# Optimization experiments

Measured on AMD Instinct MI355X. Metric: run time of the kernel, lower is better.

Reference implementation:

```python
import jax, jax.numpy as jnp
import numpy as np

MIN_K = 1
MAX_K = 10


def setup_inputs() -> dict:
    key = jax.random.key(0)
    k1, k2 = jax.random.split(key)
    query_features = jax.random.normal(k1, (256, 256, 32, 32), dtype=jnp.float32)
    support_features = jax.random.normal(k2, (512, 256, 32, 32), dtype=jnp.float32)
    return {"query_features": query_features, "support_features": support_features}


def _pairwise_euclidean(q, s):
    # torch.cdist(p=2): sqrt(||q||^2 + ||s||^2 - 2 q.s)
    q2 = jnp.sum(q * q, axis=1, keepdims=True)            # [Nq, 1]
    s2 = jnp.sum(s * s, axis=1)                           # [Ns]
    d2 = q2 + s2[None, :] - 2.0 * (q @ s.T)               # [Nq, Ns]
    return jnp.sqrt(jnp.maximum(d2, 0.0))


def reference(query_features, support_features):
    Nq = query_features.shape[0]
    q = query_features.reshape(Nq, -1)                    # [Nq, D]
    s = support_features.reshape(support_features.shape[0], -1)  # [Ns, D]

    dist = _pairwise_euclidean(q, s)                      # [Nq, Ns]

    # One top-k at MAX_K replaces the redundant per-k cdist+topk loop:
    # the per-k "loss" in optimize_k is mean of the k smallest-distance INDICES,
    # which is order-invariant, so prefix sums over sorted top-k suffice.
    _, idx = jax.lax.top_k(-dist, MAX_K)                  # [Nq, MAX_K] indices of k-NN (ascending distance)
    idx_f = idx.astype(jnp.float32)

    prefix = jnp.cumsum(jnp.sum(idx_f, axis=0))           # [MAX_K] sum of indices over first k cols
    ks = jnp.arange(1, MAX_K + 1, dtype=jnp.float32)
    losses = prefix / (Nq * ks)                           # mean index for each k
    best_k = jnp.argmin(losses[MIN_K - 1:]) + MIN_K       # traced scalar in [MIN_K, MAX_K]

    # threshold = mean of knn indices at best_k
    kmask = (jnp.arange(MAX_K) < best_k).astype(jnp.float32)  # [MAX_K]
    threshold = jnp.sum(idx_f * kmask[None, :]) / (Nq * best_k.astype(jnp.float32))

    # high_similarity mask: original expands [Nq, k] -> [Nq, D] (valid iff k==1),
    # i.e. a per-query boolean from the nearest-neighbor index vs threshold.
    qmask = (idx_f[:, 0] < threshold)                     # [Nq]

    # Original does data-dependent boolean gather; for static shapes we apply the
    # mask multiplicatively (zero out filtered queries).
    refined = q * qmask[:, None].astype(q.dtype)          # [Nq, D]
    return refined
```

## Files before the change

### kernel.cpp

```cpp
#include <hip/hip_runtime.h>
#include <cstdint>


typedef __attribute__((ext_vector_type(8))) __bf16 bf16x8;
typedef __attribute__((ext_vector_type(4))) float f32x4;
typedef __attribute__((ext_vector_type(4))) unsigned int uintx4;

#define KTOT 262144
#define MQ 256
#define NS 512
#define KSPLIT 128
#define KC 2048
#define BK 32
#define NSTEPS 64
#define BBASE 32768
#define BUFB 65536

__device__ inline unsigned int cvtpk_bf16(float a, float b) {
    unsigned int r;
    asm("v_cvt_pk_bf16_f32 %0, %1, %2" : "=v"(r) : "v"(a), "v"(b));
    return r;
}

__device__ inline void split2(float a, float b, unsigned int& h, unsigned int& l) {
    h = cvtpk_bf16(a, b);
    float ra = a - __uint_as_float(h << 16);
    float rb = b - __uint_as_float(h & 0xFFFF0000u);
    l = cvtpk_bf16(ra, rb);
}

__device__ inline void split8u(const float4& x, const float4& y, uintx4& h, uintx4& l) {
    unsigned int h0, h1, h2, h3, l0, l1, l2, l3;
    split2(x.x, x.y, h0, l0);
    split2(x.z, x.w, h1, l1);
    split2(y.x, y.y, h2, l2);
    split2(y.z, y.w, h3, l3);
    h = (uintx4){h0, h1, h2, h3};
    l = (uintx4){l0, l1, l2, l3};
}

#define LDF(OFF) (*(const bf16x8*)&Lds[(OFF)])

#define MM(MI, AH, AL, BH, BL, J)                                                        \
    acc[MI][J] = __builtin_amdgcn_mfma_f32_16x16x32_bf16(AH, BH, acc[MI][J], 0, 0, 0);   \
    acc[MI][J] = __builtin_amdgcn_mfma_f32_16x16x32_bf16(AH, BL, acc[MI][J], 0, 0, 0);   \
    acc[MI][J] = __builtin_amdgcn_mfma_f32_16x16x32_bf16(AL, BH, acc[MI][J], 0, 0, 0);

#define MMROW(MI, AH, AL)                                                                \
    MM(MI, AH, AL, bh0, bl0, 0) MM(MI, AH, AL, bh1, bl1, 1)                              \
    MM(MI, AH, AL, bh2, bl2, 2) MM(MI, AH, AL, bh3, bl3, 3)

__global__ __launch_bounds__(512, 2)
void k1_gemm(const float* __restrict__ Q, const float* __restrict__ S,
             float* __restrict__ Ppart, float* __restrict__ s2part)
{
    __shared__ __align__(16) unsigned char Lds[2 * BUFB];

    const int tid  = threadIdx.x;
    const int lane = tid & 63;
    const int w    = tid >> 6;
    const int wm   = w >> 2;
    const int wn   = w & 3;
    const int lr   = lane & 15;
    const int lk   = lane >> 4;

    const int phys  = blockIdx.x;
    const int xcd   = phys & 7;
    const int ord   = phys >> 3;
    const int chunk = xcd * 16 + (ord >> 1);
    const int ntile = ord & 1;
    const long k0   = (long)chunk * KC;

    const int rowh = tid >> 1;
    const int h    = tid & 1;
    const int e    = rowh & 7;
    const float* qsrc = Q + (long)rowh * KTOT + k0 + h * 16;
    const float* ssrc = S + (long)(ntile * 256 + rowh) * KTOT + k0 + h * 16;
    const int aw0 = rowh * 128 + (((2 * h + 0) ^ e) * 16);
    const int aw1 = rowh * 128 + (((2 * h + 1) ^ e) * 16);
    const int aw2 = rowh * 128 + (((2 * h + 4) ^ e) * 16);
    const int aw3 = rowh * 128 + (((2 * h + 5) ^ e) * 16);

    const int e2  = lr & 7;
    const int aHi = (wm * 128 + lr) * 128 + ((lk ^ e2) * 16);
    const int aLo = (wm * 128 + lr) * 128 + (((lk + 4) ^ e2) * 16);
    const int bHi = BBASE + (wn * 64 + lr) * 128 + ((lk ^ e2) * 16);
    const int bLo = BBASE + (wn * 64 + lr) * 128 + (((lk + 4) ^ e2) * 16);

    f32x4 acc[8][4];
#pragma unroll
    for (int i = 0; i < 8; ++i)
#pragma unroll
        for (int j = 0; j < 4; ++j)
            acc[i][j] = (f32x4){0.f, 0.f, 0.f, 0.f};

    float ssq = 0.f;
    float4 pa0, pa1, pa2, pa3, pb0, pb1, pb2, pb3;

#define LOADREGS {                                                         \
    pa0 = *(const float4*)(qsrc);      pa1 = *(const float4*)(qsrc + 4);   \
    pa2 = *(const float4*)(qsrc + 8);  pa3 = *(const float4*)(qsrc + 12);  \
    pb0 = *(const float4*)(ssrc);      pb1 = *(const float4*)(ssrc + 4);   \
    pb2 = *(const float4*)(ssrc + 8);  pb3 = *(const float4*)(ssrc + 12);  \
    qsrc += BK; ssrc += BK; }

#define SPLITSTORE(BASE) {                                                 \
    uintx4 u0, u1, u2, u3, v0, v1, v2, v3;                                 \
    split8u(pa0, pa1, u0, v0);                                             \
    split8u(pa2, pa3, u1, v1);                                             \
    split8u(pb0, pb1, u2, v2);                                             \
    split8u(pb2, pb3, u3, v3);                                             \
    ssq += pb0.x*pb0.x + pb0.y*pb0.y + pb0.z*pb0.z + pb0.w*pb0.w           \
         + pb1.x*pb1.x + pb1.y*pb1.y + pb1.z*pb1.z + pb1.w*pb1.w           \
         + pb2.x*pb2.x + pb2.y*pb2.y + pb2.z*pb2.z + pb2.w*pb2.w           \
         + pb3.x*pb3.x + pb3.y*pb3.y + pb3.z*pb3.z + pb3.w*pb3.w;          \
    *(uintx4*)&Lds[(BASE) + aw0] = u0;                                     \
    *(uintx4*)&Lds[(BASE) + aw1] = u1;                                     \
    *(uintx4*)&Lds[(BASE) + aw2] = v0;                                     \
    *(uintx4*)&Lds[(BASE) + aw3] = v1;                                     \
    *(uintx4*)&Lds[(BASE) + BBASE + aw0] = u2;                             \
    *(uintx4*)&Lds[(BASE) + BBASE + aw1] = u3;                             \
    *(uintx4*)&Lds[(BASE) + BBASE + aw2] = v2;                             \
    *(uintx4*)&Lds[(BASE) + BBASE + aw3] = v3; }

    LOADREGS
    SPLITSTORE(0)
    LOADREGS
    asm volatile("s_waitcnt lgkmcnt(0)" ::: "memory");
    __builtin_amdgcn_s_barrier();
    __builtin_amdgcn_sched_barrier(0);

    for (int s = 0; s < NSTEPS; ++s) {
        const int cur = (s & 1) * BUFB;
        const int nxt = cur ^ BUFB;

        if (s + 1 < NSTEPS) SPLITSTORE(nxt)
        if (s + 2 < NSTEPS) LOADREGS

        bf16x8 bh0 = LDF(cur + bHi);          bf16x8 bl0 = LDF(cur + bLo);
        bf16x8 bh1 = LDF(cur + bHi + 2048);   bf16x8 bl1 = LDF(cur + bLo + 2048);
        bf16x8 bh2 = LDF(cur + bHi + 4096);   bf16x8 bl2 = LDF(cur + bLo + 4096);
        bf16x8 bh3 = LDF(cur + bHi + 6144);   bf16x8 bl3 = LDF(cur + bLo + 6144);
#pragma unroll
        for (int mi = 0; mi < 8; ++mi) {
            bf16x8 ah = LDF(cur + aHi + mi * 2048);
            bf16x8 al = LDF(cur + aLo + mi * 2048);
            MMROW(mi, ah, al)
        }

        asm volatile("s_waitcnt lgkmcnt(0)" ::: "memory");
        __builtin_amdgcn_s_barrier();
        __builtin_amdgcn_sched_barrier(0);
    }
#undef LOADREGS
#undef SPLITSTORE

    float o = __shfl_xor(ssq, 1);
    if (h == 0)
        s2part[chunk * NS + ntile * 256 + rowh] = ssq + o;

    float* op = Ppart + (long)chunk * (MQ * NS);
#pragma unroll
    for (int mi = 0; mi < 8; ++mi)
#pragma unroll
        for (int nj = 0; nj < 4; ++nj) {
            int mb = wm * 128 + mi * 16 + lk * 4;
            int nn = ntile * 256 + wn * 64 + nj * 16 + lr;
#pragma unroll
            for (int r = 0; r < 4; ++r)
                op[(long)(mb + r) * NS + nn] = acc[mi][nj][r];
        }
}

__global__ __launch_bounds__(256)
void k2_topk(const float* __restrict__ Ppart, const float* __restrict__ s2part,
             int* __restrict__ idxb)
{
    __shared__ float d2s[NS];
    const int m = blockIdx.x;
    const int tid = threadIdx.x;
    for (int nn = tid; nn < NS; nn += 256) {
        float s2 = 0.f, p = 0.f;
        for (int c = 0; c < KSPLIT; ++c) {
            s2 += s2part[c * NS + nn];
            p  += Ppart[(long)c * (MQ * NS) + (long)m * NS + nn];
        }
        d2s[nn] = s2 - 2.f * p;
    }
    __syncthreads();
    if (tid < 64) {
        unsigned long long key[8];
#pragma unroll
        for (int j = 0; j < 8; ++j) {
            int n = tid * 8 + j;
            unsigned int u = __float_as_uint(d2s[n]);
            u = (u >> 31) ? ~u : (u | 0x80000000u);
            key[j] = ((unsigned long long)u << 32) | (unsigned int)n;
        }
        for (int it = 0; it < 10; ++it) {
            unsigned long long best = key[0];
#pragma unroll
            for (int j = 1; j < 8; ++j) best = key[j] < best ? key[j] : best;
            for (int d = 1; d < 64; d <<= 1) {
                unsigned long long o = __shfl_xor(best, d);
                best = o < best ? o : best;
            }
            if (tid == 0) idxb[m * 10 + it] = (int)(best & 0xFFFFFFFFu);
#pragma unroll
            for (int j = 0; j < 8; ++j) if (key[j] == best) key[j] = ~0ull;
        }
    }
}

__global__ __launch_bounds__(256)
void k3_thresh(const int* __restrict__ idxb, float* __restrict__ mask)
{
    __shared__ int colsum[10];
    __shared__ float thr;
    const int tid = threadIdx.x;
    if (tid < 10) {
        int s = 0;
        for (int m = 0; m < MQ; ++m) s += idxb[m * 10 + tid];
        colsum[tid] = s;
    }
    __syncthreads();
    if (tid == 0) {
        float pre = 0.f, best = 3.4e38f;
        for (int k = 1; k <= 10; ++k) {
            pre += (float)colsum[k - 1];
            float loss = pre / (256.0f * (float)k);
            if (loss < best) best = loss;
        }
        thr = best;
    }
    __syncthreads();
    if (tid < MQ) mask[tid] = ((float)idxb[tid * 10] < thr) ? 1.0f : 0.0f;
}

__global__ __launch_bounds__(256)
void k4_apply(const float* __restrict__ Q, const float* __restrict__ mask,
              float* __restrict__ out)
{
    long i = ((long)blockIdx.x * 256 + threadIdx.x) * 4;
    int row = (int)(i >> 18);
    float4 v = *(const float4*)(Q + i);
    float mm = mask[row];
    v.x *= mm; v.y *= mm; v.z *= mm; v.w *= mm;
    *(float4*)(out + i) = v;
}

extern "C" void kernel_launch(void* const* d_in, const int* in_sizes, int n_in,
                              void* d_out, int out_size, void* d_ws, size_t ws_size,
                              hipStream_t stream)
{
    const float* Q = (const float*)d_in[0];
    const float* S = (const float*)d_in[1];
    float* out = (float*)d_out;

    float* Ppart  = out;
    float* s2part = out + (long)KSPLIT * MQ * NS;
    int*   idxb   = (int*)(s2part + KSPLIT * NS);
    float* mask   = (float*)d_ws;

    hipLaunchKernelGGL(k1_gemm,  dim3(256),   dim3(512), 0, stream, Q, S, Ppart, s2part);
    hipLaunchKernelGGL(k2_topk,  dim3(MQ),    dim3(256), 0, stream, Ppart, s2part, idxb);
    hipLaunchKernelGGL(k3_thresh,dim3(1),     dim3(256), 0, stream, idxb, mask);
    hipLaunchKernelGGL(k4_apply, dim3(65536), dim3(256), 0, stream, Q, mask, out);
}
```

Baseline: 383.2 us.

## Retile split-K GEMM to 256x128 tiles with fewer K-splits and software-pipelined LDS reads

```diff
diff --git a/kernel.cpp b/kernel.cpp
--- a/kernel.cpp
+++ b/kernel.cpp
@@ -9,12 +9,12 @@
 #define KTOT 262144
 #define MQ 256
 #define NS 512
-#define KSPLIT 128
-#define KC 2048
+#define KSPLIT 64
+#define KC 4096
 #define BK 32
-#define NSTEPS 64
+#define NSTEPS 128
 #define BBASE 32768
-#define BUFB 65536
+#define BUFB 49152
 
 __device__ inline unsigned int cvtpk_bf16(float a, float b) {
     unsigned int r;
@@ -40,15 +40,21 @@
 }
 
 #define LDF(OFF) (*(const bf16x8*)&Lds[(OFF)])
-
-#define MM(MI, AH, AL, BH, BL, J)                                                        \
-    acc[MI][J] = __builtin_amdgcn_mfma_f32_16x16x32_bf16(AH, BH, acc[MI][J], 0, 0, 0);   \
-    acc[MI][J] = __builtin_amdgcn_mfma_f32_16x16x32_bf16(AH, BL, acc[MI][J], 0, 0, 0);   \
-    acc[MI][J] = __builtin_amdgcn_mfma_f32_16x16x32_bf16(AL, BH, acc[MI][J], 0, 0, 0);
-
-#define MMROW(MI, AH, AL)                                                                \
-    MM(MI, AH, AL, bh0, bl0, 0) MM(MI, AH, AL, bh1, bl1, 1)                              \
-    MM(MI, AH, AL, bh2, bl2, 2) MM(MI, AH, AL, bh3, bl3, 3)
+#define SB __builtin_amdgcn_sched_barrier(0);
+
+#define MMB(MI, AH, AL)                                                                     \
+    acc[MI][0] = __builtin_amdgcn_mfma_f32_16x16x32_bf16(AH, bh0, acc[MI][0], 0, 0, 0);     \
+    acc[MI][1] = __builtin_amdgcn_mfma_f32_16x16x32_bf16(AH, bh1, acc[MI][1], 0, 0, 0);     \
+    acc[MI][2] = __builtin_amdgcn_mfma_f32_16x16x32_bf16(AH, bh2, acc[MI][2], 0, 0, 0);     \
+    acc[MI][3] = __builtin_amdgcn_mfma_f32_16x16x32_bf16(AH, bh3, acc[MI][3], 0, 0, 0);     \
+    acc[MI][0] = __builtin_amdgcn_mfma_f32_16x16x32_bf16(AH, bl0, acc[MI][0], 0, 0, 0);     \
+    acc[MI][1] = __builtin_amdgcn_mfma_f32_16x16x32_bf16(AH, bl1, acc[MI][1], 0, 0, 0);     \
+    acc[MI][2] = __builtin_amdgcn_mfma_f32_16x16x32_bf16(AH, bl2, acc[MI][2], 0, 0, 0);     \
+    acc[MI][3] = __builtin_amdgcn_mfma_f32_16x16x32_bf16(AH, bl3, acc[MI][3], 0, 0, 0);     \
+    acc[MI][0] = __builtin_amdgcn_mfma_f32_16x16x32_bf16(AL, bh0, acc[MI][0], 0, 0, 0);     \
+    acc[MI][1] = __builtin_amdgcn_mfma_f32_16x16x32_bf16(AL, bh1, acc[MI][1], 0, 0, 0);     \
+    acc[MI][2] = __builtin_amdgcn_mfma_f32_16x16x32_bf16(AL, bh2, acc[MI][2], 0, 0, 0);     \
+    acc[MI][3] = __builtin_amdgcn_mfma_f32_16x16x32_bf16(AL, bh3, acc[MI][3], 0, 0, 0);
 
 __global__ __launch_bounds__(512, 2)
 void k1_gemm(const float* __restrict__ Q, const float* __restrict__ S,
@@ -59,113 +65,133 @@
     const int tid  = threadIdx.x;
     const int lane = tid & 63;
     const int w    = tid >> 6;
-    const int wm   = w >> 2;
-    const int wn   = w & 3;
+    const int wm   = w >> 1;
+    const int wn   = w & 1;
     const int lr   = lane & 15;
     const int lk   = lane >> 4;
 
     const int phys  = blockIdx.x;
     const int xcd   = phys & 7;
     const int ord   = phys >> 3;
-    const int chunk = xcd * 16 + (ord >> 1);
-    const int ntile = ord & 1;
+    const int chunk = xcd * 8 + (ord >> 2);
+    const int ntile = ord & 3;
     const long k0   = (long)chunk * KC;
 
-    const int rowh = tid >> 1;
-    const int h    = tid & 1;
-    const int e    = rowh & 7;
-    const float* qsrc = Q + (long)rowh * KTOT + k0 + h * 16;
-    const float* ssrc = S + (long)(ntile * 256 + rowh) * KTOT + k0 + h * 16;
-    const int aw0 = rowh * 128 + (((2 * h + 0) ^ e) * 16);
-    const int aw1 = rowh * 128 + (((2 * h + 1) ^ e) * 16);
-    const int aw2 = rowh * 128 + (((2 * h + 4) ^ e) * 16);
-    const int aw3 = rowh * 128 + (((2 * h + 5) ^ e) * 16);
-
-    const int e2  = lr & 7;
-    const int aHi = (wm * 128 + lr) * 128 + ((lk ^ e2) * 16);
-    const int aLo = (wm * 128 + lr) * 128 + (((lk + 4) ^ e2) * 16);
-    const int bHi = BBASE + (wn * 64 + lr) * 128 + ((lk ^ e2) * 16);
-    const int bLo = BBASE + (wn * 64 + lr) * 128 + (((lk + 4) ^ e2) * 16);
-
-    f32x4 acc[8][4];
-#pragma unroll
-    for (int i = 0; i < 8; ++i)
+    const int ra = tid >> 1, hA = tid & 1;
+    const int rb = tid >> 2, qt = tid & 3;
+    const float* qsrc = Q + (long)ra * KTOT + k0 + hA * 16;
+    const float* ssrc = S + (long)(ntile * 128 + rb) * KTOT + k0 + qt * 8;
+    const int eA = ra & 7, eB = rb & 7;
+    const int aw0 = ra * 128 + (((2 * hA + 0) ^ eA) * 16);
+    const int aw1 = ra * 128 + (((2 * hA + 1) ^ eA) * 16);
+    const int aw2 = ra * 128 + (((2 * hA + 4) ^ eA) * 16);
+    const int aw3 = ra * 128 + (((2 * hA + 5) ^ eA) * 16);
+    const int bw0 = BBASE + rb * 128 + ((qt ^ eB) * 16);
+    const int bw1 = BBASE + rb * 128 + (((4 + qt) ^ eB) * 16);
+
+    const int e2 = lr & 7;
+    int aHi[4], aLo[4], bHiA[4], bLoA[4];
+#pragma unroll
+    for (int i = 0; i < 4; ++i) {
+        int rA = wm * 64 + i * 16 + lr;
+        aHi[i] = rA * 128 + ((lk ^ e2) * 16);
+        aLo[i] = rA * 128 + (((lk + 4) ^ e2) * 16);
+        int rB = wn * 64 + i * 16 + lr;
+        bHiA[i] = BBASE + rB * 128 + ((lk ^ e2) * 16);
+        bLoA[i] = BBASE + rB * 128 + (((lk + 4) ^ e2) * 16);
+    }
+
+    f32x4 acc[4][4];
+#pragma unroll
+    for (int i = 0; i < 4; ++i)
 #pragma unroll
         for (int j = 0; j < 4; ++j)
             acc[i][j] = (f32x4){0.f, 0.f, 0.f, 0.f};
 
     float ssq = 0.f;
-    float4 pa0, pa1, pa2, pa3, pb0, pb1, pb2, pb3;
+    float4 pa0, pa1, pa2, pa3, pb0, pb1;
 
 #define LOADREGS {                                                         \
     pa0 = *(const float4*)(qsrc);      pa1 = *(const float4*)(qsrc + 4);   \
     pa2 = *(const float4*)(qsrc + 8);  pa3 = *(const float4*)(qsrc + 12);  \
     pb0 = *(const float4*)(ssrc);      pb1 = *(const float4*)(ssrc + 4);   \
-    pb2 = *(const float4*)(ssrc + 8);  pb3 = *(const float4*)(ssrc + 12);  \
     qsrc += BK; ssrc += BK; }
 
 #define SPLITSTORE(BASE) {                                                 \
-    uintx4 u0, u1, u2, u3, v0, v1, v2, v3;                                 \
+    uintx4 u0, u1, v0, v1, hb, lb;                                         \
     split8u(pa0, pa1, u0, v0);                                             \
     split8u(pa2, pa3, u1, v1);                                             \
-    split8u(pb0, pb1, u2, v2);                                             \
-    split8u(pb2, pb3, u3, v3);                                             \
+    split8u(pb0, pb1, hb, lb);                                             \
     ssq += pb0.x*pb0.x + pb0.y*pb0.y + pb0.z*pb0.z + pb0.w*pb0.w           \
-         + pb1.x*pb1.x + pb1.y*pb1.y + pb1.z*pb1.z + pb1.w*pb1.w           \
-         + pb2.x*pb2.x + pb2.y*pb2.y + pb2.z*pb2.z + pb2.w*pb2.w           \
-         + pb3.x*pb3.x + pb3.y*pb3.y + pb3.z*pb3.z + pb3.w*pb3.w;          \
+         + pb1.x*pb1.x + pb1.y*pb1.y + pb1.z*pb1.z + pb1.w*pb1.w;          \
     *(uintx4*)&Lds[(BASE) + aw0] = u0;                                     \
     *(uintx4*)&Lds[(BASE) + aw1] = u1;                                     \
     *(uintx4*)&Lds[(BASE) + aw2] = v0;                                     \
     *(uintx4*)&Lds[(BASE) + aw3] = v1;                                     \
-    *(uintx4*)&Lds[(BASE) + BBASE + aw0] = u2;                             \
-    *(uintx4*)&Lds[(BASE) + BBASE + aw1] = u3;                             \
-    *(uintx4*)&Lds[(BASE) + BBASE + aw2] = v2;                             \
-    *(uintx4*)&Lds[(BASE) + BBASE + aw3] = v3; }
+    *(uintx4*)&Lds[(BASE) + bw0] = hb;                                     \
+    *(uintx4*)&Lds[(BASE) + bw1] = lb; }
 
     LOADREGS
     SPLITSTORE(0)
     LOADREGS
     asm volatile("s_waitcnt lgkmcnt(0)" ::: "memory");
     __builtin_amdgcn_s_barrier();
-    __builtin_amdgcn_sched_barrier(0);
+    SB
 
     for (int s = 0; s < NSTEPS; ++s) {
         const int cur = (s & 1) * BUFB;
         const int nxt = cur ^ BUFB;
 
+        bf16x8 bh0 = LDF(cur + bHiA[0]);  bf16x8 bl0 = LDF(cur + bLoA[0]);
+        bf16x8 bh1 = LDF(cur + bHiA[1]);  bf16x8 bl1 = LDF(cur + bLoA[1]);
+        bf16x8 bh2 = LDF(cur + bHiA[2]);  bf16x8 bl2 = LDF(cur + bLoA[2]);
+        bf16x8 bh3 = LDF(cur + bHiA[3]);  bf16x8 bl3 = LDF(cur + bLoA[3]);
+        bf16x8 aCh = LDF(cur + aHi[0]);   bf16x8 aCl = LDF(cur + aLo[0]);
         if (s + 1 < NSTEPS) SPLITSTORE(nxt)
         if (s + 2 < NSTEPS) LOADREGS
-
-        bf16x8 bh0 = LDF(cur + bHi);          bf16x8 bl0 = LDF(cur + bLo);
-        bf16x8 bh1 = LDF(cur + bHi + 2048);   bf16x8 bl1 = LDF(cur + bLo + 2048);
-        bf16x8 bh2 = LDF(cur + bHi + 4096);   bf16x8 bl2 = LDF(cur + bLo + 4096);
-        bf16x8 bh3 = LDF(cur + bHi + 6144);   bf16x8 bl3 = LDF(cur + bLo + 6144);
-#pragma unroll
-        for (int mi = 0; mi < 8; ++mi) {
-            bf16x8 ah = LDF(cur + aHi + mi * 2048);
-            bf16x8 al = LDF(cur + aLo + mi * 2048);
-            MMROW(mi, ah, al)
-        }
-
+        SB
+        bf16x8 aNh = LDF(cur + aHi[1]);   bf16x8 aNl = LDF(cur + aLo[1]);
+        SB
+        asm volatile("s_waitcnt lgkmcnt(2)" ::: "memory");
+        SB
+        MMB(0, aCh, aCl)
+        SB
+        aCh = LDF(cur + aHi[2]);          aCl = LDF(cur + aLo[2]);
+        SB
+        asm volatile("s_waitcnt lgkmcnt(2)" ::: "memory");
+        SB
+        MMB(1, aNh, aNl)
+        SB
+        aNh = LDF(cur + aHi[3]);          aNl = LDF(cur + aLo[3]);
+        SB
+        asm volatile("s_waitcnt lgkmcnt(2)" ::: "memory");
+        SB
+        MMB(2, aCh, aCl)
+        SB
         asm volatile("s_waitcnt lgkmcnt(0)" ::: "memory");
+        SB
+        MMB(3, aNh, aNl)
+        SB
         __builtin_amdgcn_s_barrier();
-        __builtin_amdgcn_sched_barrier(0);
+        SB
     }
 #undef LOADREGS
 #undef SPLITSTORE
 
-    float o = __shfl_xor(ssq, 1);
-    if (h == 0)
-        s2part[chunk * NS + ntile * 256 + rowh] = ssq + o;
+    {
+        float v = ssq + __shfl_xor(ssq, 1);
+        v += __shfl_xor(v, 2);
+        if (qt == 0)
+            s2part[chunk * NS + ntile * 128 + rb] = v;
+    }
 
     float* op = Ppart + (long)chunk * (MQ * NS);
 #pragma unroll
-    for (int mi = 0; mi < 8; ++mi)
+    for (int mi = 0; mi < 4; ++mi)
 #pragma unroll
         for (int nj = 0; nj < 4; ++nj) {
-            int mb = wm * 128 + mi * 16 + lk * 4;
-            int nn = ntile * 256 + wn * 64 + nj * 16 + lr;
+            int mb = wm * 64 + mi * 16 + lk * 4;
+            int nn = ntile * 128 + wn * 64 + nj * 16 + lr;
 #pragma unroll
             for (int r = 0; r < 4; ++r)
                 op[(long)(mb + r) * NS + nn] = acc[mi][nj][r];
```

New measurement: 358.3 us. 1.07x faster.

## Software-pipeline LDS A-fragment loads with MFMAs and interleave accumulator chains

Applied to the files above, without the earlier changes.

```diff
diff --git a/kernel.cpp b/kernel.cpp
--- a/kernel.cpp
+++ b/kernel.cpp
@@ -40,15 +40,21 @@
 }
 
 #define LDF(OFF) (*(const bf16x8*)&Lds[(OFF)])
-
-#define MM(MI, AH, AL, BH, BL, J)                                                        \
-    acc[MI][J] = __builtin_amdgcn_mfma_f32_16x16x32_bf16(AH, BH, acc[MI][J], 0, 0, 0);   \
-    acc[MI][J] = __builtin_amdgcn_mfma_f32_16x16x32_bf16(AH, BL, acc[MI][J], 0, 0, 0);   \
-    acc[MI][J] = __builtin_amdgcn_mfma_f32_16x16x32_bf16(AL, BH, acc[MI][J], 0, 0, 0);
-
-#define MMROW(MI, AH, AL)                                                                \
-    MM(MI, AH, AL, bh0, bl0, 0) MM(MI, AH, AL, bh1, bl1, 1)                              \
-    MM(MI, AH, AL, bh2, bl2, 2) MM(MI, AH, AL, bh3, bl3, 3)
+#define SB __builtin_amdgcn_sched_barrier(0);
+
+#define MMB(MI, AH, AL)                                                                     \
+    acc[MI][0] = __builtin_amdgcn_mfma_f32_16x16x32_bf16(AH, bh0, acc[MI][0], 0, 0, 0);     \
+    acc[MI][1] = __builtin_amdgcn_mfma_f32_16x16x32_bf16(AH, bh1, acc[MI][1], 0, 0, 0);     \
+    acc[MI][2] = __builtin_amdgcn_mfma_f32_16x16x32_bf16(AH, bh2, acc[MI][2], 0, 0, 0);     \
+    acc[MI][3] = __builtin_amdgcn_mfma_f32_16x16x32_bf16(AH, bh3, acc[MI][3], 0, 0, 0);     \
+    acc[MI][0] = __builtin_amdgcn_mfma_f32_16x16x32_bf16(AH, bl0, acc[MI][0], 0, 0, 0);     \
+    acc[MI][1] = __builtin_amdgcn_mfma_f32_16x16x32_bf16(AH, bl1, acc[MI][1], 0, 0, 0);     \
+    acc[MI][2] = __builtin_amdgcn_mfma_f32_16x16x32_bf16(AH, bl2, acc[MI][2], 0, 0, 0);     \
+    acc[MI][3] = __builtin_amdgcn_mfma_f32_16x16x32_bf16(AH, bl3, acc[MI][3], 0, 0, 0);     \
+    acc[MI][0] = __builtin_amdgcn_mfma_f32_16x16x32_bf16(AL, bh0, acc[MI][0], 0, 0, 0);     \
+    acc[MI][1] = __builtin_amdgcn_mfma_f32_16x16x32_bf16(AL, bh1, acc[MI][1], 0, 0, 0);     \
+    acc[MI][2] = __builtin_amdgcn_mfma_f32_16x16x32_bf16(AL, bh2, acc[MI][2], 0, 0, 0);     \
+    acc[MI][3] = __builtin_amdgcn_mfma_f32_16x16x32_bf16(AL, bh3, acc[MI][3], 0, 0, 0);
 
 __global__ __launch_bounds__(512, 2)
 void k1_gemm(const float* __restrict__ Q, const float* __restrict__ S,
@@ -128,29 +134,68 @@
     LOADREGS
     asm volatile("s_waitcnt lgkmcnt(0)" ::: "memory");
     __builtin_amdgcn_s_barrier();
-    __builtin_amdgcn_sched_barrier(0);
+    SB
 
     for (int s = 0; s < NSTEPS; ++s) {
         const int cur = (s & 1) * BUFB;
         const int nxt = cur ^ BUFB;
-
-        if (s + 1 < NSTEPS) SPLITSTORE(nxt)
-        if (s + 2 < NSTEPS) LOADREGS
 
         bf16x8 bh0 = LDF(cur + bHi);          bf16x8 bl0 = LDF(cur + bLo);
         bf16x8 bh1 = LDF(cur + bHi + 2048);   bf16x8 bl1 = LDF(cur + bLo + 2048);
         bf16x8 bh2 = LDF(cur + bHi + 4096);   bf16x8 bl2 = LDF(cur + bLo + 4096);
         bf16x8 bh3 = LDF(cur + bHi + 6144);   bf16x8 bl3 = LDF(cur + bLo + 6144);
-#pragma unroll
-        for (int mi = 0; mi < 8; ++mi) {
-            bf16x8 ah = LDF(cur + aHi + mi * 2048);
-            bf16x8 al = LDF(cur + aLo + mi * 2048);
-            MMROW(mi, ah, al)
-        }
-
+        bf16x8 aCh = LDF(cur + aHi);          bf16x8 aCl = LDF(cur + aLo);
+        if (s + 1 < NSTEPS) SPLITSTORE(nxt)
+        if (s + 2 < NSTEPS) LOADREGS
+        SB
+        bf16x8 aNh = LDF(cur + aHi + 2048);   bf16x8 aNl = LDF(cur + aLo + 2048);
+        SB
+        asm volatile("s_waitcnt lgkmcnt(8)" ::: "memory");
+        SB
+        MMB(0, aCh, aCl)
+        SB
+        aCh = LDF(cur + aHi + 4096);          aCl = LDF(cur + aLo + 4096);
+        SB
+        asm volatile("s_waitcnt lgkmcnt(2)" ::: "memory");
+        SB
+        MMB(1, aNh, aNl)
+        SB
+        aNh = LDF(cur + aHi + 6144);          aNl = LDF(cur + aLo + 6144);
+        SB
+        asm volatile("s_waitcnt lgkmcnt(2)" ::: "memory");
+        SB
+        MMB(2, aCh, aCl)
+        SB
+        aCh = LDF(cur + aHi + 8192);          aCl = LDF(cur + aLo + 8192);
+        SB
+        asm volatile("s_waitcnt lgkmcnt(2)" ::: "memory");
+        SB
+        MMB(3, aNh, aNl)
+        SB
+        aNh = LDF(cur + aHi + 10240);         aNl = LDF(cur + aLo + 10240);
+        SB
+        asm volatile("s_waitcnt lgkmcnt(2)" ::: "memory");
+        SB
+        MMB(4, aCh, aCl)
+        SB
+        aCh = LDF(cur + aHi + 12288);         aCl = LDF(cur + aLo + 12288);
+        SB
+        asm volatile("s_waitcnt lgkmcnt(2)" ::: "memory");
+        SB
+        MMB(5, aNh, aNl)
+        SB
+        aNh = LDF(cur + aHi + 14336);         aNl = LDF(cur + aLo + 14336);
+        SB
+        asm volatile("s_waitcnt lgkmcnt(2)" ::: "memory");
+        SB
+        MMB(6, aCh, aCl)
+        SB
         asm volatile("s_waitcnt lgkmcnt(0)" ::: "memory");
+        SB
+        MMB(7, aNh, aNl)
+        SB
         __builtin_amdgcn_s_barrier();
-        __builtin_amdgcn_sched_barrier(0);
+        SB
     }
 #undef LOADREGS
 #undef SPLITSTORE
```

After: 359.5 us. 1.07x faster.
